# Kernel optimization log

Hardware: AMD Instinct MI355X
Metric: run time of the kernel (lower is better)

Reference implementation:

```python
import jax, jax.numpy as jnp
import numpy as np

K = 17
PAD = K // 2
THRESHOLD = 55.0
TEMPERATURE = 20.0


def _normalize_0_100(x, eps=1e-8):
    x_min = jnp.min(x)
    x_max = jnp.max(x)
    return 100.0 * (x - x_min) / jnp.maximum(x_max - x_min, eps)


def setup_inputs() -> dict:
    key = jax.random.key(0)
    k1, k2, k3, k4 = jax.random.split(key, 4)
    H_total, W_total = 512, 512
    Fdim, Odim = 100, 180
    f_print1 = jax.random.uniform(k1, (H_total, W_total), dtype=jnp.float32)
    freq_ind = jax.random.randint(k2, (H_total, W_total), 0, Fdim)
    orient_ind = jax.random.randint(k3, (H_total, W_total), 0, Odim)
    filterbank = jax.random.normal(k4, (Fdim, Odim, K, K), dtype=jnp.float32)
    return {
        "f_print1": f_print1,
        "freq_ind": freq_ind,
        "orient_ind": orient_ind,
        "filterbank": filterbank,
        "H": 480,
        "W": 480,
        "margin": 32,
    }


def reference(f_print1, freq_ind, orient_ind, filterbank, H, W, margin):
    Fdim, Odim, K1, K2 = filterbank.shape
    H_total, W_total = f_print1.shape
    # im2col: zero-padded sliding KxK windows, row-major over the kernel window
    # (matches torch F.unfold ordering for a single channel)
    x_pad = jnp.pad(f_print1, PAD)
    ih = jnp.arange(H_total)[:, None] + jnp.arange(K)[None, :]  # (H_total, K)
    iw = jnp.arange(W_total)[:, None] + jnp.arange(K)[None, :]  # (W_total, K)
    patches = x_pad[ih[:, None, :, None], iw[None, :, None, :]]  # (H,W,K,K)

    # per-pixel kernel gather (indices are 1-based in the source, clamped)
    f0 = jnp.clip(freq_ind - 1, 0, Fdim - 1)
    o0 = jnp.clip(orient_ind - 1, 0, Odim - 1)
    idx = f0 * Odim + o0  # (H,W)
    kernels = filterbank.reshape(Fdim * Odim, K, K)[idx]  # (H,W,K,K)

    # spatially-varying convolution: per-pixel multiply + reduce
    y = jnp.einsum('hwkl,hwkl->hw', patches, kernels)

    out = _normalize_0_100(y)
    out = 100.0 * jax.nn.sigmoid(TEMPERATURE * (out / 100.0 - THRESHOLD / 100.0))
    out = _normalize_0_100(out)
    return out
```

## Files before the change

kernel.cpp:

```cpp
#include <hip/hip_runtime.h>
#include <math.h>

#define FDIM  100
#define ODIM  180
#define HTOT  512
#define WTOT  512
#define TILE  32
#define REG   48
#define LDSW  49
#define NSLICE 8
#define SLICE_SZ 2250
#define NTILE 256
#define NBLK  (NTILE * NSLICE)
#define TEMPERATURE 20.0f
#define THRESHOLD   55.0f

typedef float f32x4 __attribute__((ext_vector_type(4)));


template <int CTRL>
__device__ __forceinline__ float dpp_ror_add(float v) {
    const int r = __builtin_amdgcn_mov_dpp(__float_as_int(v), CTRL, 0xf, 0xf, false);
    return v + __int_as_float(r);
}

__global__ __launch_bounds__(256) void filter_sliced(
    const float* __restrict__ x,
    const int*   __restrict__ freq,
    const int*   __restrict__ orient,
    const float* __restrict__ fb,
    float*       __restrict__ y,
    float2*      __restrict__ partial)
{
    __shared__ float tile[REG][LDSW];
    __shared__ int   sel[TILE * TILE];
    __shared__ unsigned int nsel;

    const int gid   = blockIdx.x;
    const int slice = gid & (NSLICE - 1);
    const int t     = gid >> 3;
    const int bx    = t & 15, by = t >> 4;
    const int tid   = threadIdx.x;
    const int lane  = tid & 63;

    if (tid == 0) nsel = 0;
    __syncthreads();

    const int lo = slice * SLICE_SZ;
    #pragma unroll
    for (int k = 0; k < 4; ++k) {
        const int p  = tid + k * 256;
        const int pr = p >> 5, pc = p & 31;
        const int pid = (by * TILE + pr) * WTOT + bx * TILE + pc;
        int f0 = freq[pid] - 1;
        int o0 = orient[pid] - 1;
        f0 = f0 < 0 ? 0 : (f0 > FDIM - 1 ? FDIM - 1 : f0);
        o0 = o0 < 0 ? 0 : (o0 > ODIM - 1 ? ODIM - 1 : o0);
        const int idx = f0 * ODIM + o0;
        const bool want = (idx >= lo && idx < lo + SLICE_SZ);
        const unsigned long long mask = __ballot(want);
        unsigned int base = 0;
        if (lane == 0) base = atomicAdd(&nsel, (unsigned int)__popcll(mask));
        base = __shfl(base, 0, 64);
        if (want) {
            const int pos = __popcll(mask & ((1ULL << lane) - 1ULL));
            sel[base + pos] = (idx << 10) | p;
        }
    }

    const int h0 = by * TILE - 8;
    const int w0 = bx * TILE - 8;
    for (int i = tid; i < REG * REG; i += 256) {
        const int r = i / REG, c = i - r * REG;
        const int gh = h0 + r, gw = w0 + c;
        float v = 0.f;
        if (gh >= 0 && gh < HTOT && gw >= 0 && gw < WTOT)
            v = x[gh * WTOT + gw];
        tile[r][c] = v;
    }
    __syncthreads();

    const unsigned int m = nsel;
    const int l  = tid & 15;
    const int qw = tid >> 4;

    int offs[18];
    #pragma unroll
    for (int j = 0; j < 18; ++j) {
        const int e = j * 16 + l;
        offs[j] = (e / 17) * LDSW + (e % 17);
    }

    float mn = 3.4e38f, mx = -3.4e38f;

    for (unsigned int s = qw; s < m; s += 16) {
        const int packed = sel[s];
        const int tp  = packed & 1023;
        const int ppy = tp >> 5, ppx = tp & 31;
        const float* __restrict__ kf = fb + (size_t)(packed >> 10) * 289;

        float kv[18];
        #pragma unroll
        for (int j = 0; j < 18; ++j) kv[j] = kf[j * 16 + l];
        const float kt = kf[288];

        const float* __restrict__ base = &tile[ppy][ppx];
        float a0 = 0.f, a1 = 0.f, a2 = 0.f, a3 = 0.f;
        #pragma unroll
        for (int j = 0; j < 16; j += 4) {
            a0 = fmaf(kv[j    ], base[offs[j    ]], a0);
            a1 = fmaf(kv[j + 1], base[offs[j + 1]], a1);
            a2 = fmaf(kv[j + 2], base[offs[j + 2]], a2);
            a3 = fmaf(kv[j + 3], base[offs[j + 3]], a3);
        }
        a0 = fmaf(kv[16], base[offs[16]], a0);
        a1 = fmaf(kv[17], base[offs[17]], a1);
        float acc = (a0 + a1) + (a2 + a3);
        if (l == 0) acc = fmaf(kt, base[16 * LDSW + 16], acc);

        acc = dpp_ror_add<0x128>(acc);
        acc = dpp_ror_add<0x124>(acc);
        acc = dpp_ror_add<0x122>(acc);
        acc = dpp_ror_add<0x121>(acc);

        if (l == 0)
            y[(by * TILE + ppy) * WTOT + bx * TILE + ppx] = acc;
        mn = fminf(mn, acc);
        mx = fmaxf(mx, acc);
    }

    #pragma unroll
    for (int off = 32; off > 0; off >>= 1) {
        mn = fminf(mn, __shfl_down(mn, off, 64));
        mx = fmaxf(mx, __shfl_down(mx, off, 64));
    }
    __shared__ float smn[4], smx[4];
    const int wid = tid >> 6;
    if (lane == 0) { smn[wid] = mn; smx[wid] = mx; }
    __syncthreads();
    if (tid == 0) {
        float bmn = smn[0], bmx = smx[0];
        #pragma unroll
        for (int i = 1; i < 4; ++i) {
            bmn = fminf(bmn, smn[i]);
            bmx = fmaxf(bmx, smx[i]);
        }
        partial[gid] = make_float2(bmn, bmx);
    }
}

__global__ __launch_bounds__(256) void filter_final(
    float* __restrict__ y,
    const float2* __restrict__ partial)
{
    const int tid = threadIdx.x;
    float mn = 3.4e38f, mx = -3.4e38f;
    for (int i = tid; i < NBLK; i += 256) {
        const float2 p = partial[i];
        mn = fminf(mn, p.x);
        mx = fmaxf(mx, p.y);
    }
    #pragma unroll
    for (int off = 32; off > 0; off >>= 1) {
        mn = fminf(mn, __shfl_down(mn, off, 64));
        mx = fmaxf(mx, __shfl_down(mx, off, 64));
    }
    __shared__ float smn[4], smx[4];
    const int wid = tid >> 6, lane = tid & 63;
    if (lane == 0) { smn[wid] = mn; smx[wid] = mx; }
    __syncthreads();
    __shared__ float sfin[2];
    if (tid == 0) {
        float bmn = smn[0], bmx = smx[0];
        #pragma unroll
        for (int i = 1; i < 4; ++i) {
            bmn = fminf(bmn, smn[i]);
            bmx = fmaxf(bmx, smx[i]);
        }
        sfin[0] = bmn; sfin[1] = bmx;
    }
    __syncthreads();

    const float ymin = sfin[0];
    const float rng  = fmaxf(sfin[1] - ymin, 1e-8f);
    const float smin = 100.f / (1.f + expf( 11.f));
    const float smax = 100.f / (1.f + expf(-9.f));
    const float srng = fmaxf(smax - smin, 1e-8f);

    const int base = blockIdx.x * 1024 + tid * 4;
    f32x4 v = *reinterpret_cast<const f32x4*>(&y[base]);
    #pragma unroll
    for (int i = 0; i < 4; ++i) {
        const float o1 = 100.f * (v[i] - ymin) / rng;
        const float s  = 100.f / (1.f + expf(-(TEMPERATURE * (o1 * 0.01f - THRESHOLD * 0.01f))));
        v[i] = 100.f * (s - smin) / srng;
    }
    *reinterpret_cast<f32x4*>(&y[base]) = v;
}

extern "C" void kernel_launch(void* const* d_in, const int* in_sizes, int n_in,
                              void* d_out, int out_size, void* d_ws, size_t ws_size,
                              hipStream_t stream) {
    const float* x      = (const float*)d_in[0];
    const int*   freq   = (const int*)d_in[1];
    const int*   orient = (const int*)d_in[2];
    const float* fb     = (const float*)d_in[3];
    float*       out    = (float*)d_out;
    float2*      partial = (float2*)d_ws;

    filter_sliced<<<dim3(NBLK), 256, 0, stream>>>(x, freq, orient, fb, out, partial);

    filter_final<<<(HTOT * WTOT) / 1024, 256, 0, stream>>>(out, partial);
}
```

Measured before the change: 32.86 us.

## Remap patch-kernel lane mapping to row/column form and pad LDS to limit occupancy

Replaces the precomputed per-lane offset table with a row-major mapping: each of 16 lanes handles one column of the 16 leading rows, plus one element of the last column and the corner tap. This drops the 18 offset registers and uses simple strided LDS addressing instead of irregular gathers, though global kernel-weight loads become strided by 17 floats. It also adds an unused LDS pad array, referenced under a condition that never holds, so the compiler keeps it and blocks per CU are capped. That cap is meant to cut cache thrashing or contention, at the cost of less latency hiding.

```diff
diff --git a/kernel.cpp b/kernel.cpp
--- a/kernel.cpp
+++ b/kernel.cpp
@@ -34,6 +34,7 @@
 {
     __shared__ float tile[REG][LDSW];
     __shared__ int   sel[TILE * TILE];
+    __shared__ float occupancy_pad[1100];
     __shared__ unsigned int nsel;
 
     const int gid   = blockIdx.x;
@@ -84,13 +85,6 @@
     const int l  = tid & 15;
     const int qw = tid >> 4;
 
-    int offs[18];
-    #pragma unroll
-    for (int j = 0; j < 18; ++j) {
-        const int e = j * 16 + l;
-        offs[j] = (e / 17) * LDSW + (e % 17);
-    }
-
     float mn = 3.4e38f, mx = -3.4e38f;
 
     for (unsigned int s = qw; s < m; s += 16) {
@@ -98,25 +92,30 @@
         const int tp  = packed & 1023;
         const int ppy = tp >> 5, ppx = tp & 31;
         const float* __restrict__ kf = fb + (size_t)(packed >> 10) * 289;
-
-        float kv[18];
-        #pragma unroll
-        for (int j = 0; j < 18; ++j) kv[j] = kf[j * 16 + l];
-        const float kt = kf[288];
-
-        const float* __restrict__ base = &tile[ppy][ppx];
+        const float* __restrict__ bp = &tile[ppy][ppx];
+
+        float kv[17];
+        #pragma unroll
+        for (int r = 0; r < 17; ++r) kv[r] = kf[17 * r + l];
+        const float kc   = kf[17 * l + 16];
+        const float k288 = kf[288];
+
         float a0 = 0.f, a1 = 0.f, a2 = 0.f, a3 = 0.f;
         #pragma unroll
-        for (int j = 0; j < 16; j += 4) {
-            a0 = fmaf(kv[j    ], base[offs[j    ]], a0);
-            a1 = fmaf(kv[j + 1], base[offs[j + 1]], a1);
-            a2 = fmaf(kv[j + 2], base[offs[j + 2]], a2);
-            a3 = fmaf(kv[j + 3], base[offs[j + 3]], a3);
-        }
-        a0 = fmaf(kv[16], base[offs[16]], a0);
-        a1 = fmaf(kv[17], base[offs[17]], a1);
+        for (int r = 0; r < 16; r += 2) {
+            const float p0 = bp[r * LDSW + l];
+            const float p1 = bp[r * LDSW + LDSW + l];
+            a0 = fmaf(kv[r],     p0, a0);
+            a1 = fmaf(kv[r + 1], p1, a1);
+        }
+        a2 = fmaf(kv[16], bp[16 * LDSW + l], a2);
+        {
+            const float q0 = bp[l * LDSW + 16];
+            const float q1 = bp[l * LDSW + LDSW + 16];
+            a2 = fmaf(kc, q0, a2);
+            a3 = fmaf((l == 15) ? k288 : 0.f, q1, a3);
+        }
         float acc = (a0 + a1) + (a2 + a3);
-        if (l == 0) acc = fmaf(kt, base[16 * LDSW + 16], acc);
 
         acc = dpp_ror_add<0x128>(acc);
         acc = dpp_ror_add<0x124>(acc);
@@ -128,6 +127,8 @@
         mn = fminf(mn, acc);
         mx = fmaxf(mx, acc);
     }
+
+    if (m > 1024u) tile[0][0] += occupancy_pad[tid];
 
     #pragma unroll
     for (int off = 32; off > 0; off >>= 1) {
```

Result: no change. 33.31 us (+1.4%).
